# Kernel tuning notes

Measured on AMD Instinct MI355X. Metric: run time of the kernel, lower is better.

Reference implementation:

```python
import jax, jax.numpy as jnp
import numpy as np

B = 2048
S = 8            # mem_slots
H = 8            # num_heads
HS = 128         # head_size
KS = 128         # key_size (= head_size)
VS = 128         # value_size
M = H * HS       # mem_size = 1024
QKV = 2 * KS + VS            # 384
TOTAL = QKV * H              # 3072
IN_DIM = 1024
NUM_GATES = 2                # gate_style='memory' -> gate size 1, x2 gates
FORGET_BIAS = 1.0
INPUT_BIAS = 0.0


def _glorot(key, shape):
    fan_in, fan_out = shape[0], shape[1]
    lim = np.sqrt(6.0 / (fan_in + fan_out))
    return jax.random.uniform(key, shape, jnp.float32, -lim, lim)


def setup_inputs() -> dict:
    key = jax.random.key(0)
    ks = jax.random.split(key, 16)
    return {
        "inputs": jax.random.normal(ks[0], (B, IN_DIM), jnp.float32),
        "memory": jax.random.normal(ks[1], (B, S * M), jnp.float32),
        "kernel_qkv": _glorot(ks[2], (M, TOTAL)),
        "bias_qkv": jnp.zeros((TOTAL,), jnp.float32),
        "kernel_gi": _glorot(ks[3], (M, NUM_GATES)),
        "bias_gi": _glorot(ks[4], (1, NUM_GATES))[0],
        "kernel_gm": _glorot(ks[5], (M, NUM_GATES)),
        "bias_gm": _glorot(ks[6], (1, NUM_GATES))[0],
        "kernel_in": _glorot(ks[7], (IN_DIM, M)),
        "bias_in": _glorot(ks[8], (1, M))[0],
        "mlp_k0": _glorot(ks[9], (M, M)),
        "mlp_b0": _glorot(ks[10], (1, M))[0],
        "mlp_k1": _glorot(ks[11], (M, M)),
        "mlp_b1": _glorot(ks[12], (1, M))[0],
    }


def reference(inputs, memory, kernel_qkv, bias_qkv, kernel_gi, bias_gi,
              kernel_gm, bias_gm, kernel_in, bias_in,
              mlp_k0, mlp_b0, mlp_k1, mlp_b1):
    b = inputs.shape[0]
    mem = memory.reshape(b, S, M)                       # (B, S, M)
    x = inputs @ kernel_in + bias_in                    # (B, M)
    mpi = jnp.concatenate([mem, x[:, None, :]], axis=1)  # (B, S+1, M)

    # multi-head attention over memory + input slot
    qkv = (mpi @ kernel_qkv + bias_qkv).reshape(b, S + 1, H, QKV)
    qkv = qkv.transpose(0, 2, 1, 3)                     # (B, H, S+1, QKV)
    q = qkv[..., :KS] * (QKV ** -0.5)
    k = qkv[..., KS:2 * KS]
    v = qkv[..., 2 * KS:]
    w = jax.nn.softmax(jnp.einsum('bhqd,bhkd->bhqk', q, k), axis=-1)
    att = jnp.einsum('bhqk,bhkd->bhqd', w, v)           # (B, H, S+1, VS)
    att = att.transpose(0, 2, 1, 3).reshape(b, S + 1, M)
    m1 = mpi + att                                      # residual attention

    # residual 2-layer MLP (relu between layers)
    h = jax.nn.relu(m1 @ mlp_k0 + mlp_b0)
    m2 = m1 + (h @ mlp_k1 + mlp_b1)

    nxt = m2[:, :-1, :]                                 # drop input slot

    # per-slot (memory-style) gates
    gi = (x @ kernel_gi + bias_gi)[:, None, :]          # (B, 1, 2)
    gm = jnp.tanh(mem) @ kernel_gm + bias_gm            # (B, S, 2)
    gates = gm + gi
    input_gate = jax.nn.sigmoid(gates[..., :1] + INPUT_BIAS)
    forget_gate = jax.nn.sigmoid(gates[..., 1:] + FORGET_BIAS)

    nxt = input_gate * jnp.tanh(nxt) + forget_gate * mem
    return nxt.reshape(b, S * M)
```

## Files before the change

kernel.cpp:

```cpp
#include <hip/hip_runtime.h>
#include <math.h>


typedef unsigned short ushort_t;
typedef short bf16x8_t __attribute__((ext_vector_type(8)));
typedef float f32x4_t  __attribute__((ext_vector_type(4)));

#define MFMA16(a, b, c) __builtin_amdgcn_mfma_f32_16x16x32_bf16((a), (b), (c), 0, 0, 0)

__device__ __forceinline__ ushort_t f2bf(float f) {
    unsigned int u = __float_as_uint(f);
    u += 0x7fff + ((u >> 16) & 1);
    return (ushort_t)(u >> 16);
}
__device__ __forceinline__ float bf2f(ushort_t h) {
    return __uint_as_float(((unsigned int)h) << 16);
}
__device__ __forceinline__ float fast_tanh(float x) {
    float e = __expf(2.0f * x);
    return 1.0f - 2.0f * __builtin_amdgcn_rcpf(e + 1.0f);
}
__device__ __forceinline__ float fast_sigmoid(float x) {
    return __builtin_amdgcn_rcpf(1.0f + __expf(-x));
}

__device__ __forceinline__ void load_lds_16(const void* g, void* l) {
    __builtin_amdgcn_global_load_lds(
        (const __attribute__((address_space(1))) void*)g,
        (__attribute__((address_space(3))) void*)l, 16, 0, 0);
}

__global__ __launch_bounds__(256)
void gemm128db(const ushort_t* __restrict__ A, const ushort_t* __restrict__ Wt,
               const float* __restrict__ bias, float* __restrict__ Cf,
               ushort_t* __restrict__ Cb, const ushort_t* __restrict__ resb,
               const float* __restrict__ igfg, const ushort_t* __restrict__ memb,
               float* __restrict__ outp, int N, int K, int relu,
               int ncol, int nrow)
{
    __shared__ __align__(16) ushort_t As[2][128][32];
    __shared__ __align__(16) ushort_t Bs[2][128][32];
    const int tid  = threadIdx.x;
    const int wave = tid >> 6, lane = tid & 63;
    const int wr = (wave >> 1) * 64;
    const int wc = (wave & 1)  * 64;
    const int lrow  = lane & 15;
    const int lquad = lane >> 4;

    int l = blockIdx.x, rT, cT;
    if ((nrow & 7) == 0) {
        int group = l / (8 * ncol);
        int w     = l - group * 8 * ncol;
        rT = group * 8 + (w & 7);
        cT = w >> 3;
    } else {
        rT = l / ncol;
        cT = l - rT * ncol;
    }
    const int rowBase = rT * 128;
    const int colBase = cT * 128;

    auto stage = [&](const ushort_t* __restrict__ G, int gbase, int k0,
                     ushort_t (*lds)[32]) {
        #pragma unroll
        for (int i = 0; i < 2; ++i) {
            int e   = i * 256 + tid;
            int row = e >> 2;
            int sl  = e & 3;
            int gc  = sl ^ ((row >> 1) & 3);
            const ushort_t* g = G + (size_t)(gbase + row) * K + k0 + gc * 8;
            load_lds_16(g, &lds[row][sl * 8]);
        }
    };

    f32x4_t acc[4][4] = {};

    stage(A,  rowBase, 0, As[0]);
    stage(Wt, colBase, 0, Bs[0]);
    __syncthreads();

    int buf = 0;
    for (int k0 = 0; k0 < K; k0 += 32) {
        if (k0 + 32 < K) {
            stage(A,  rowBase, k0 + 32, As[buf ^ 1]);
            stage(Wt, colBase, k0 + 32, Bs[buf ^ 1]);
        }

        bf16x8_t af[4], bfr[4];
        #pragma unroll
        for (int t = 0; t < 4; ++t) {
            int ma = wr + t * 16 + lrow;
            int pa = lquad ^ ((ma >> 1) & 3);
            af[t]  = *(const bf16x8_t*)&As[buf][ma][pa * 8];
            int nb = wc + t * 16 + lrow;
            int pb = lquad ^ ((nb >> 1) & 3);
            bfr[t] = *(const bf16x8_t*)&Bs[buf][nb][pb * 8];
        }
        #pragma unroll
        for (int mi = 0; mi < 4; ++mi)
            #pragma unroll
            for (int ni = 0; ni < 4; ++ni)
                acc[mi][ni] = MFMA16(af[mi], bfr[ni], acc[mi][ni]);

        __syncthreads();
        buf ^= 1;
    }

    #pragma unroll
    for (int mi = 0; mi < 4; ++mi) {
        #pragma unroll
        for (int ni = 0; ni < 4; ++ni) {
            int col = colBase + wc + ni * 16 + lrow;
            float bv = bias[col];
            #pragma unroll
            for (int r = 0; r < 4; ++r) {
                int row = rowBase + wr + mi * 16 + lquad * 4 + r;
                size_t idx = (size_t)row * N + col;
                float v = acc[mi][ni][r] + bv;
                if (resb) v += bf2f(resb[idx]);
                if (relu) v = fmaxf(v, 0.f);
                if (outp) {
                    float ig = igfg[row * 2], fg = igfg[row * 2 + 1];
                    float mv = bf2f(memb[(size_t)(row + (row >> 3)) * N + col]);
                    outp[idx] = ig * fast_tanh(v) + fg * mv;
                } else if (Cb) {
                    Cb[idx] = f2bf(v);
                } else {
                    Cf[idx] = v;
                }
            }
        }
    }
}

__global__ __launch_bounds__(512, 2)
void gemm256(const ushort_t* __restrict__ A, const ushort_t* __restrict__ Wt,
             const float* __restrict__ bias, ushort_t* __restrict__ Cb,
             int N, int K, int ncol, int nrow)
{
    __shared__ __align__(16) ushort_t As[2][256][64];
    __shared__ __align__(16) ushort_t Bs[2][256][64];

    const int tid   = threadIdx.x;
    const int wave  = tid >> 6, lane = tid & 63;
    const int lrow  = lane & 15, lquad = lane >> 4;
    const int wr    = (wave >> 2) * 64;
    const int wc    = (wave & 3) * 32;

    const int nwg = ncol * nrow;
    int l = blockIdx.x;
    int q = nwg >> 3, r = nwg & 7;
    int xcd = l & 7, ib = l >> 3;
    int wg = (xcd < r) ? xcd * (q + 1) + ib : r * (q + 1) + (xcd - r) * q + ib;
    int rT = wg / ncol, cT = wg - rT * ncol;
    const int rowBase = rT * 256;
    const int colBase = cT * 256;

    const int NT = K >> 6;

    auto stage = [&](const ushort_t* __restrict__ G, int gbase, int kt,
                     int half, ushort_t (*lds)[64]) {
        #pragma unroll
        for (int j = 0; j < 2; ++j) {
            int ci   = j * 512 + tid;
            int rl   = ci >> 3;
            int slot = ci & 7;
            int row  = half * 128 + rl;
            int gc   = slot ^ (rl & 7);
            const ushort_t* g = G + (size_t)(gbase + row) * K + kt * 64 + gc * 8;
            load_lds_16(g, &lds[row][slot * 8]);
        }
    };

    stage(A,  rowBase, 0, 0, As[0]);
    stage(A,  rowBase, 0, 1, As[0]);
    stage(Wt, colBase, 0, 0, Bs[0]);
    stage(Wt, colBase, 0, 1, Bs[0]);
    asm volatile("" ::: "memory");
    stage(A,  rowBase, 1, 0, As[1]);
    stage(Wt, colBase, 1, 0, Bs[1]);
    asm volatile("s_waitcnt vmcnt(4)" ::: "memory");
    __builtin_amdgcn_s_barrier();

    f32x4_t acc[8][4] = {};
    bf16x8_t af[4][2], bfr[4][2];
    const int s0 = (lquad ^ (lrow & 7)) * 8;
    const int s1 = ((lquad ^ (lrow & 7)) ^ 4) * 8;

    for (int t = 0; t < NT; ++t) {
        const int bf = t & 1, nf = bf ^ 1;
        ushort_t (*Ab)[64] = As[bf];
        ushort_t (*Bb)[64] = Bs[bf];

        #pragma unroll
        for (int m = 0; m < 4; ++m) {
            int ra = wr + m * 16 + lrow;
            af[m][0] = *(const bf16x8_t*)&Ab[ra][s0];
            af[m][1] = *(const bf16x8_t*)&Ab[ra][s1];
        }
        #pragma unroll
        for (int n = 0; n < 2; ++n) {
            int rb = wc + n * 16 + lrow;
            bfr[n][0] = *(const bf16x8_t*)&Bb[rb][s0];
            bfr[n][1] = *(const bf16x8_t*)&Bb[rb][s1];
        }
        if (t + 1 < NT) stage(A, rowBase, t + 1, 1, As[nf]);
        __builtin_amdgcn_s_barrier();
        asm volatile("s_waitcnt lgkmcnt(0)" ::: "memory");
        __builtin_amdgcn_s_setprio(1);
        #pragma unroll
        for (int m = 0; m < 4; ++m)
            #pragma unroll
            for (int n = 0; n < 2; ++n) {
                acc[m][n] = MFMA16(af[m][0], bfr[n][0], acc[m][n]);
                acc[m][n] = MFMA16(af[m][1], bfr[n][1], acc[m][n]);
            }
        __builtin_amdgcn_s_setprio(0);
        __builtin_amdgcn_s_barrier();

        #pragma unroll
        for (int n = 0; n < 2; ++n) {
            int rb = 128 + wc + n * 16 + lrow;
            bfr[2 + n][0] = *(const bf16x8_t*)&Bb[rb][s0];
            bfr[2 + n][1] = *(const bf16x8_t*)&Bb[rb][s1];
        }
        if (t + 1 < NT) stage(Wt, colBase, t + 1, 1, Bs[nf]);
        __builtin_amdgcn_s_barrier();
        asm volatile("s_waitcnt lgkmcnt(0)" ::: "memory");
        __builtin_amdgcn_s_setprio(1);
        #pragma unroll
        for (int m = 0; m < 4; ++m)
            #pragma unroll
            for (int n = 0; n < 2; ++n) {
                acc[m][2 + n] = MFMA16(af[m][0], bfr[2 + n][0], acc[m][2 + n]);
                acc[m][2 + n] = MFMA16(af[m][1], bfr[2 + n][1], acc[m][2 + n]);
            }
        __builtin_amdgcn_s_setprio(0);
        __builtin_amdgcn_s_barrier();

        #pragma unroll
        for (int m = 0; m < 4; ++m) {
            int ra = 128 + wr + m * 16 + lrow;
            af[m][0] = *(const bf16x8_t*)&Ab[ra][s0];
            af[m][1] = *(const bf16x8_t*)&Ab[ra][s1];
        }
        if (t + 2 < NT) stage(A, rowBase, t + 2, 0, As[bf]);
        __builtin_amdgcn_s_barrier();
        asm volatile("s_waitcnt lgkmcnt(0)" ::: "memory");
        __builtin_amdgcn_s_setprio(1);
        #pragma unroll
        for (int m = 0; m < 4; ++m)
            #pragma unroll
            for (int n = 0; n < 2; ++n) {
                acc[4 + m][n] = MFMA16(af[m][0], bfr[n][0], acc[4 + m][n]);
                acc[4 + m][n] = MFMA16(af[m][1], bfr[n][1], acc[4 + m][n]);
            }
        __builtin_amdgcn_s_setprio(0);
        __builtin_amdgcn_s_barrier();

        if (t + 2 < NT) {
            stage(Wt, colBase, t + 2, 0, Bs[bf]);
            asm volatile("s_waitcnt vmcnt(4)" ::: "memory");
        } else if (t + 1 < NT) {
            asm volatile("s_waitcnt vmcnt(0)" ::: "memory");
        }
        __builtin_amdgcn_s_barrier();
        __builtin_amdgcn_s_setprio(1);
        #pragma unroll
        for (int m = 0; m < 4; ++m)
            #pragma unroll
            for (int n = 0; n < 2; ++n) {
                acc[4 + m][2 + n] = MFMA16(af[m][0], bfr[2 + n][0], acc[4 + m][2 + n]);
                acc[4 + m][2 + n] = MFMA16(af[m][1], bfr[2 + n][1], acc[4 + m][2 + n]);
            }
        __builtin_amdgcn_s_setprio(0);
        __builtin_amdgcn_s_barrier();
    }

    #pragma unroll
    for (int mi = 0; mi < 8; ++mi) {
        #pragma unroll
        for (int ni = 0; ni < 4; ++ni) {
            int col = colBase + wc + (ni & 1) * 16 + ((ni >> 1) << 7) + lrow;
            float bv = bias[col];
            #pragma unroll
            for (int rr = 0; rr < 4; ++rr) {
                int row = rowBase + wr + (mi & 3) * 16 + ((mi >> 2) << 7)
                        + lquad * 4 + rr;
                size_t idx = (size_t)row * N + col;
                Cb[idx] = f2bf(acc[mi][ni][rr] + bv);
            }
        }
    }
}

__global__ __launch_bounds__(256)
void conv_bf16(const float* __restrict__ in, ushort_t* __restrict__ out, size_t n)
{
    size_t i = ((size_t)blockIdx.x * 256 + threadIdx.x) * 4;
    if (i >= n) return;
    float4 v = *(const float4*)(in + i);
    out[i + 0] = f2bf(v.x); out[i + 1] = f2bf(v.y);
    out[i + 2] = f2bf(v.z); out[i + 3] = f2bf(v.w);
}

__global__ __launch_bounds__(256)
void conv_wt4(const float* __restrict__ W0, ushort_t* __restrict__ T0,
              const float* __restrict__ W1, ushort_t* __restrict__ T1,
              const float* __restrict__ W2, ushort_t* __restrict__ T2,
              const float* __restrict__ W3, ushort_t* __restrict__ T3)
{
    __shared__ float t[32][33];
    int bx = blockIdx.x;
    const float* W; ushort_t* T; int N;
    if (bx < 32)       { W = W0; T = T0; N = 1024; }
    else if (bx < 128) { W = W1; T = T1; N = 3072; bx -= 32; }
    else if (bx < 160) { W = W2; T = T2; N = 1024; bx -= 128; }
    else               { W = W3; T = T3; N = 1024; bx -= 160; }
    const int K = 1024;
    const int n0 = bx * 32, k0 = blockIdx.y * 32;
    const int tx = threadIdx.x & 31, ty = threadIdx.x >> 5;
    #pragma unroll
    for (int i = 0; i < 4; ++i)
        t[ty * 4 + i][tx] = W[(size_t)(k0 + ty * 4 + i) * N + n0 + tx];
    __syncthreads();
    #pragma unroll
    for (int i = 0; i < 4; ++i)
        T[(size_t)(n0 + ty * 4 + i) * K + k0 + tx] = f2bf(t[tx][ty * 4 + i]);
}

__global__ __launch_bounds__(256)
void prep_kernel(const float* __restrict__ mem, const ushort_t* __restrict__ xb,
                 const float* __restrict__ kgm, const float* __restrict__ bgm,
                 const float* __restrict__ gi, ushort_t* __restrict__ mpi,
                 float* __restrict__ igfg)
{
    const int row = blockIdx.x;
    const int tid = threadIdx.x;
    const int b = row / 9, s = row - b * 9;
    if (s == 8) {
        ((ushort4*)(mpi + (size_t)row * 1024))[tid] =
            ((const ushort4*)(xb + (size_t)b * 1024))[tid];
        return;
    }
    const float* mrow = mem + ((size_t)b * 8 + s) * 1024;
    float4 v = ((const float4*)mrow)[tid];
    ushort4 o;
    o.x = f2bf(v.x); o.y = f2bf(v.y); o.z = f2bf(v.z); o.w = f2bf(v.w);
    ((ushort4*)(mpi + (size_t)row * 1024))[tid] = o;
    float4 k0 = ((const float4*)kgm)[tid * 2];
    float4 k1 = ((const float4*)kgm)[tid * 2 + 1];
    float t0 = fast_tanh(v.x), t1 = fast_tanh(v.y);
    float t2 = fast_tanh(v.z), t3 = fast_tanh(v.w);
    float g0 = t0 * k0.x + t1 * k0.z + t2 * k1.x + t3 * k1.z;
    float g1 = t0 * k0.y + t1 * k0.w + t2 * k1.y + t3 * k1.w;
    #pragma unroll
    for (int m = 1; m <= 32; m <<= 1) {
        g0 += __shfl_xor(g0, m);
        g1 += __shfl_xor(g1, m);
    }
    __shared__ float wg[4][2];
    if ((tid & 63) == 0) { wg[tid >> 6][0] = g0; wg[tid >> 6][1] = g1; }
    __syncthreads();
    if (tid == 0) {
        float G0 = wg[0][0] + wg[1][0] + wg[2][0] + wg[3][0];
        float G1 = wg[0][1] + wg[1][1] + wg[2][1] + wg[3][1];
        int orow = b * 8 + s;
        igfg[orow * 2 + 0] = fast_sigmoid(G0 + bgm[0] + gi[b * 2 + 0]);
        igfg[orow * 2 + 1] = fast_sigmoid(G1 + bgm[1] + gi[b * 2 + 1] + 1.0f);
    }
}

__global__ __launch_bounds__(256)
void attn_kernel(const ushort_t* __restrict__ qkv, const ushort_t* __restrict__ mpib,
                 ushort_t* __restrict__ m1b)
{
    const int bh = blockIdx.x;
    const int b = bh >> 3, h = bh & 7;
    constexpr int VS = 40;
    __shared__ __align__(16) ushort_t vt[128 * VS];
    __shared__ __align__(16) ushort_t pw[16 * VS];
    const int tid  = threadIdx.x;
    const int lane = tid & 63, wave = tid >> 6;
    const int quad = lane >> 4;
    const size_t qrow0 = (size_t)b * 9;

    {
        unsigned long long* z = (unsigned long long*)vt;
        #pragma unroll
        for (int i = 0; i < 5; ++i) z[tid + i * 256] = 0ull;
        if (tid < 160) ((unsigned long long*)pw)[tid] = 0ull;
    }
    __syncthreads();
    for (int c = tid; c < 9 * 128; c += 256) {
        int j = c >> 7, d = c & 127;
        vt[d * VS + j] = qkv[(qrow0 + j) * 3072 + (size_t)h * 384 + 256 + d];
    }

    f32x4_t sacc = {0.f, 0.f, 0.f, 0.f};
    if (wave == 0) {
        const int m  = lane & 7;
        const int n  = lane & 15;
        const int nc = n > 8 ? 8 : n;
        const ushort_t* qb = qkv + (qrow0 + m)  * 3072 + (size_t)h * 384 + quad * 8;
        const ushort_t* kb = qkv + (qrow0 + nc) * 3072 + (size_t)h * 384 + 128 + quad * 8;
        #pragma unroll
        for (int t = 0; t < 4; ++t) {
            bf16x8_t aq = *(const bf16x8_t*)(qb + t * 32);
            bf16x8_t bk = *(const bf16x8_t*)(kb + t * 32);
            sacc = __builtin_amdgcn_mfma_f32_16x16x32_bf16(aq, bk, sacc, 0, 0, 0);
        }
    }
    __syncthreads();

    if (wave == 0) {
        const int j = lane & 15;
        const float scale = 0.05103103630798288f;
        #pragma unroll
        for (int r = 0; r < 4; ++r) {
            float sv = (j < 9) ? sacc[r] * scale : -1e30f;
            float mx = sv;
            mx = fmaxf(mx, __shfl_xor(mx, 1));
            mx = fmaxf(mx, __shfl_xor(mx, 2));
            mx = fmaxf(mx, __shfl_xor(mx, 4));
            mx = fmaxf(mx, __shfl_xor(mx, 8));
            float e = (j < 9) ? __expf(sv - mx) : 0.f;
            float sum = e;
            sum += __shfl_xor(sum, 1);
            sum += __shfl_xor(sum, 2);
            sum += __shfl_xor(sum, 4);
            sum += __shfl_xor(sum, 8);
            pw[(quad * 4 + r) * VS + j] = f2bf(e * __builtin_amdgcn_rcpf(sum));
        }
    }
    __syncthreads();

    {
        const int n  = lane & 15;
        const int d0 = wave * 32;
        bf16x8_t pa = *(const bf16x8_t*)&pw[n * VS + quad * 8];
        #pragma unroll
        for (int g = 0; g < 2; ++g) {
            int d = d0 + g * 16 + n;
            bf16x8_t vb = *(const bf16x8_t*)&vt[d * VS + quad * 8];
            f32x4_t o = {0.f, 0.f, 0.f, 0.f};
            o = __builtin_amdgcn_mfma_f32_16x16x32_bf16(pa, vb, o, 0, 0, 0);
            #pragma unroll
            for (int r = 0; r < 4; ++r) {
                int i = quad * 4 + r;
                if (i < 8) {
                    float mv = bf2f(mpib[((size_t)b * 9 + i) * 1024 + (size_t)h * 128 + d]);
                    size_t idx = ((size_t)b * 8 + i) * 1024 + (size_t)h * 128 + d;
                    m1b[idx] = f2bf(o[r] + mv);
                }
            }
        }
    }
}

__global__ __launch_bounds__(256)
void gi_kernel(const ushort_t* __restrict__ xb, const float* __restrict__ kgi,
               const float* __restrict__ bgi, float* __restrict__ gi)
{
    const int b = blockIdx.x, tid = threadIdx.x;
    float g0 = 0.f, g1 = 0.f;
    for (int k = tid; k < 1024; k += 256) {
        float xv = bf2f(xb[(size_t)b * 1024 + k]);
        g0 += xv * kgi[k * 2];
        g1 += xv * kgi[k * 2 + 1];
    }
    #pragma unroll
    for (int m = 1; m <= 32; m <<= 1) {
        g0 += __shfl_xor(g0, m);
        g1 += __shfl_xor(g1, m);
    }
    __shared__ float wg[4][2];
    if ((tid & 63) == 0) { wg[tid >> 6][0] = g0; wg[tid >> 6][1] = g1; }
    __syncthreads();
    if (tid == 0) {
        gi[b * 2 + 0] = wg[0][0] + wg[1][0] + wg[2][0] + wg[3][0] + bgi[0];
        gi[b * 2 + 1] = wg[0][1] + wg[1][1] + wg[2][1] + wg[3][1] + bgi[1];
    }
}

extern "C" void kernel_launch(void* const* d_in, const int* in_sizes, int n_in,
                              void* d_out, int out_size, void* d_ws, size_t ws_size,
                              hipStream_t stream)
{
    const float* inputs     = (const float*)d_in[0];
    const float* memory     = (const float*)d_in[1];
    const float* kernel_qkv = (const float*)d_in[2];
    const float* bias_qkv   = (const float*)d_in[3];
    const float* kernel_gi  = (const float*)d_in[4];
    const float* bias_gi    = (const float*)d_in[5];
    const float* kernel_gm  = (const float*)d_in[6];
    const float* bias_gm    = (const float*)d_in[7];
    const float* kernel_in  = (const float*)d_in[8];
    const float* bias_in    = (const float*)d_in[9];
    const float* mlp_k0     = (const float*)d_in[10];
    const float* mlp_b0     = (const float*)d_in[11];
    const float* mlp_k1     = (const float*)d_in[12];
    const float* mlp_b1     = (const float*)d_in[13];
    float* out = (float*)d_out;

    char* p = (char*)d_ws;
    ushort_t* in_b   = (ushort_t*)p;  p += (size_t)2048 * 1024 * 2;
    ushort_t* x_b    = (ushort_t*)p;  p += (size_t)2048 * 1024 * 2;
    ushort_t* wt_in  = (ushort_t*)p;  p += (size_t)1024 * 1024 * 2;
    ushort_t* wt_qkv = (ushort_t*)p;  p += (size_t)3072 * 1024 * 2;
    ushort_t* wt_k0  = (ushort_t*)p;  p += (size_t)1024 * 1024 * 2;
    ushort_t* wt_k1  = (ushort_t*)p;  p += (size_t)1024 * 1024 * 2;
    float*    ws_gi  = (float*)p;     p += (size_t)2048 * 2 * 4;
    float*    igfg   = (float*)p;     p += (size_t)16384 * 2 * 4;
    ushort_t* ws_mpi = (ushort_t*)p;  p += (size_t)18432 * 1024 * 2;
    ushort_t* m1b    = (ushort_t*)p;  p += (size_t)16384 * 1024 * 2;
    ushort_t* ws_h   = (ushort_t*)p;  p += (size_t)16384 * 1024 * 2;
    size_t fixed = (size_t)(p - (char*)d_ws);

    int Bc = 256;
    for (int cand = 1024; cand >= 256; cand >>= 1)
        if (fixed + (size_t)cand * 9 * 3072 * 2 <= ws_size) { Bc = cand; break; }
    ushort_t* ws_qkv = (ushort_t*)p;

    conv_bf16<<<2048, 256, 0, stream>>>(inputs, in_b, (size_t)2048 * 1024);
    conv_wt4<<<dim3(192, 32), 256, 0, stream>>>(
        kernel_in, wt_in, kernel_qkv, wt_qkv, mlp_k0, wt_k0, mlp_k1, wt_k1);

    gemm128db<<<16 * 8, 256, 0, stream>>>(
        in_b, wt_in, bias_in, nullptr, x_b, nullptr, nullptr, nullptr, nullptr,
        1024, 1024, 0, 8, 16);

    gi_kernel<<<2048, 256, 0, stream>>>(x_b, kernel_gi, bias_gi, ws_gi);
    prep_kernel<<<18432, 256, 0, stream>>>(memory, x_b, kernel_gm, bias_gm,
                                           ws_gi, ws_mpi, igfg);

    const int NC = 2048 / Bc;
    for (int c = 0; c < NC; ++c) {
        const int b0 = c * Bc;
        const int nrow = Bc * 9 / 256;
        gemm256<<<12 * nrow, 512, 0, stream>>>(
            ws_mpi + (size_t)b0 * 9 * 1024, wt_qkv, bias_qkv, ws_qkv,
            3072, 1024, 12, nrow);
        attn_kernel<<<Bc * 8, 256, 0, stream>>>(
            ws_qkv, ws_mpi + (size_t)b0 * 9 * 1024, m1b + (size_t)b0 * 8192);
    }

    gemm128db<<<128 * 8, 256, 0, stream>>>(
        m1b, wt_k0, mlp_b0, nullptr, ws_h, nullptr, nullptr, nullptr, nullptr,
        1024, 1024, 1, 8, 128);

    gemm128db<<<128 * 8, 256, 0, stream>>>(
        ws_h, wt_k1, mlp_b1, nullptr, nullptr, m1b, igfg, ws_mpi, out,
        1024, 1024, 0, 8, 128);
}
```

Measured before the change: 550.7 us.

## Triple-buffer LDS pipeline in 128x128 GEMM with explicit vmcnt waits

Replaces the double-buffered K loop of the 128x128 bf16 GEMM with a three-stage LDS ring. Each iteration waits on vmcnt counters, reads its fragments, then issues the async global-to-LDS load for tile t+3 before running the MFMAs. The aim is to keep more global loads in flight and hide memory latency behind compute in the MLP and input-projection GEMMs. It uses 50% more LDS per block, adds a launch-bounds hint for three blocks per CU, and relies on hand-written waitcnt values that must match the number of loads each thread issues.

New measurement: 547.7 us. About the same (-0.5%).

```diff
diff --git a/kernel.cpp b/kernel.cpp
--- a/kernel.cpp
+++ b/kernel.cpp
@@ -30,16 +30,16 @@
         (__attribute__((address_space(3))) void*)l, 16, 0, 0);
 }
 
-__global__ __launch_bounds__(256)
-void gemm128db(const ushort_t* __restrict__ A, const ushort_t* __restrict__ Wt,
+__global__ __launch_bounds__(256, 3)
+void gemm128p3(const ushort_t* __restrict__ A, const ushort_t* __restrict__ Wt,
                const float* __restrict__ bias, float* __restrict__ Cf,
                ushort_t* __restrict__ Cb, const ushort_t* __restrict__ resb,
                const float* __restrict__ igfg, const ushort_t* __restrict__ memb,
                float* __restrict__ outp, int N, int K, int relu,
                int ncol, int nrow)
 {
-    __shared__ __align__(16) ushort_t As[2][128][32];
-    __shared__ __align__(16) ushort_t Bs[2][128][32];
+    __shared__ __align__(16) ushort_t As[3][128][32];
+    __shared__ __align__(16) ushort_t Bs[3][128][32];
     const int tid  = threadIdx.x;
     const int wave = tid >> 6, lane = tid & 63;
     const int wr = (wave >> 1) * 64;
@@ -60,50 +60,65 @@
     const int rowBase = rT * 128;
     const int colBase = cT * 128;
 
-    auto stage = [&](const ushort_t* __restrict__ G, int gbase, int k0,
-                     ushort_t (*lds)[32]) {
+    auto stage = [&](int k0, int b) {
         #pragma unroll
         for (int i = 0; i < 2; ++i) {
             int e   = i * 256 + tid;
-            int row = e >> 2;
-            int sl  = e & 3;
+            int row = e >> 2, sl = e & 3;
             int gc  = sl ^ ((row >> 1) & 3);
-            const ushort_t* g = G + (size_t)(gbase + row) * K + k0 + gc * 8;
-            load_lds_16(g, &lds[row][sl * 8]);
+            load_lds_16(A + (size_t)(rowBase + row) * K + k0 + gc * 8,
+                        &As[b][row][sl * 8]);
+        }
+        #pragma unroll
+        for (int i = 0; i < 2; ++i) {
+            int e   = i * 256 + tid;
+            int row = e >> 2, sl = e & 3;
+            int gc  = sl ^ ((row >> 1) & 3);
+            load_lds_16(Wt + (size_t)(colBase + row) * K + k0 + gc * 8,
+                        &Bs[b][row][sl * 8]);
         }
     };
 
+    const int NT = K >> 5;
+
+    stage(0, 0);
+    asm volatile("" ::: "memory");
+    if (NT > 1) stage(32, 1);
+    asm volatile("" ::: "memory");
+    if (NT > 2) stage(64, 2);
+
     f32x4_t acc[4][4] = {};
 
-    stage(A,  rowBase, 0, As[0]);
-    stage(Wt, colBase, 0, Bs[0]);
-    __syncthreads();
-
-    int buf = 0;
-    for (int k0 = 0; k0 < K; k0 += 32) {
-        if (k0 + 32 < K) {
-            stage(A,  rowBase, k0 + 32, As[buf ^ 1]);
-            stage(Wt, colBase, k0 + 32, Bs[buf ^ 1]);
-        }
+    for (int t = 0; t < NT; ++t) {
+        const int b = t % 3;
+        if (t + 2 < NT)
+            asm volatile("s_waitcnt vmcnt(8)" ::: "memory");
+        else if (t + 1 < NT)
+            asm volatile("s_waitcnt vmcnt(4)" ::: "memory");
+        else
+            asm volatile("s_waitcnt vmcnt(0)" ::: "memory");
+        __builtin_amdgcn_s_barrier();
 
         bf16x8_t af[4], bfr[4];
         #pragma unroll
-        for (int t = 0; t < 4; ++t) {
-            int ma = wr + t * 16 + lrow;
+        for (int q = 0; q < 4; ++q) {
+            int ma = wr + q * 16 + lrow;
             int pa = lquad ^ ((ma >> 1) & 3);
-            af[t]  = *(const bf16x8_t*)&As[buf][ma][pa * 8];
-            int nb = wc + t * 16 + lrow;
+            af[q]  = *(const bf16x8_t*)&As[b][ma][pa * 8];
+            int nb = wc + q * 16 + lrow;
             int pb = lquad ^ ((nb >> 1) & 3);
-            bfr[t] = *(const bf16x8_t*)&Bs[buf][nb][pb * 8];
-        }
+            bfr[q] = *(const bf16x8_t*)&Bs[b][nb][pb * 8];
+        }
+        asm volatile("s_waitcnt lgkmcnt(0)" ::: "memory");
+        __builtin_amdgcn_s_barrier();
+        __builtin_amdgcn_sched_barrier(0);
+        if (t + 3 < NT) stage((t + 3) * 32, b);
+
         #pragma unroll
         for (int mi = 0; mi < 4; ++mi)
             #pragma unroll
             for (int ni = 0; ni < 4; ++ni)
                 acc[mi][ni] = MFMA16(af[mi], bfr[ni], acc[mi][ni]);
-
-        __syncthreads();
-        buf ^= 1;
     }
 
     #pragma unroll
@@ -526,7 +541,7 @@
     conv_wt4<<<dim3(192, 32), 256, 0, stream>>>(
         kernel_in, wt_in, kernel_qkv, wt_qkv, mlp_k0, wt_k0, mlp_k1, wt_k1);
 
-    gemm128db<<<16 * 8, 256, 0, stream>>>(
+    gemm128p3<<<16 * 8, 256, 0, stream>>>(
         in_b, wt_in, bias_in, nullptr, x_b, nullptr, nullptr, nullptr, nullptr,
         1024, 1024, 0, 8, 16);
 
@@ -545,11 +560,11 @@
             ws_qkv, ws_mpi + (size_t)b0 * 9 * 1024, m1b + (size_t)b0 * 8192);
     }
 
-    gemm128db<<<128 * 8, 256, 0, stream>>>(
+    gemm128p3<<<128 * 8, 256, 0, stream>>>(
         m1b, wt_k0, mlp_b0, nullptr, ws_h, nullptr, nullptr, nullptr, nullptr,
         1024, 1024, 1, 8, 128);
 
-    gemm128db<<<128 * 8, 256, 0, stream>>>(
+    gemm128p3<<<128 * 8, 256, 0, stream>>>(
         ws_h, wt_k1, mlp_b1, nullptr, nullptr, m1b, igfg, ws_mpi, out,
         1024, 1024, 0, 8, 128);
 }
```
